# Kernel optimization log

Measured on AMD Instinct MI355X. Metric: run time of the kernel, lower is better.

Reference implementation:

```python
import jax, jax.numpy as jnp
import numpy as np

N, D, R, E, H = 100000, 128, 4, 150000, 8
DK = D // H  # 16


def setup_inputs() -> dict:
    key = jax.random.key(0)
    ks = jax.random.split(key, 12)
    w_scale = 1.0 / np.sqrt(D)
    rel_scale = 1.0 / np.sqrt(DK)
    return {
        'x': jax.random.normal(ks[0], (N, D), dtype=jnp.float32),
        'edges_src': jax.random.randint(ks[1], (R, E), 0, N, dtype=jnp.int32),
        'edges_dst': jax.random.randint(ks[2], (R, E), 0, N, dtype=jnp.int32),
        'Wk': jax.random.normal(ks[3], (D, D), dtype=jnp.float32) * w_scale,
        'bk': jnp.zeros((D,), dtype=jnp.float32),
        'Wq': jax.random.normal(ks[4], (D, D), dtype=jnp.float32) * w_scale,
        'bq': jnp.zeros((D,), dtype=jnp.float32),
        'Wv': jax.random.normal(ks[5], (D, D), dtype=jnp.float32) * w_scale,
        'bv': jnp.zeros((D,), dtype=jnp.float32),
        'Wa': jax.random.normal(ks[6], (D, D), dtype=jnp.float32) * w_scale,
        'ba': jnp.zeros((D,), dtype=jnp.float32),
        'rel_att': jax.random.normal(ks[7], (R, H, DK, DK), dtype=jnp.float32) * rel_scale,
        'rel_msg': jax.random.normal(ks[8], (R, H, DK, DK), dtype=jnp.float32) * rel_scale,
        'rel_pri': jnp.ones((R, H), dtype=jnp.float32),
        'skip': jnp.ones((1,), dtype=jnp.float32),
    }


def reference(x, edges_src, edges_dst, Wk, bk, Wq, bq, Wv, bv, Wa, ba,
              rel_att, rel_msg, rel_pri, skip):
    n, d = x.shape
    r, e = edges_src.shape
    h, dk = rel_att.shape[1], rel_att.shape[2]
    sqrt_dk = jnp.sqrt(jnp.asarray(dk, dtype=x.dtype))

    # per-type k/q/v projections (single node type) -> [N, H, dk]
    k = (x @ Wk.T + bk).reshape(n, h, dk)
    q = (x @ Wq.T + bq).reshape(n, h, dk)
    v = (x @ Wv.T + bv).reshape(n, h, dk)

    # edge_attention: per-relation per-head dk x dk transforms on gathered src feats
    key_e = jnp.einsum('rehd,rhdf->rehf', k[edges_src], rel_att)   # [R,E,H,dk]
    att = (q[edges_dst] * key_e).sum(-1) * rel_pri[:, None, :] / sqrt_dk  # [R,E,H]
    val = jnp.einsum('rehd,rhdf->rehf', v[edges_src], rel_msg)     # [R,E,H,dk]

    # mailbox softmax per (relation, dst node, head) via segment ops
    seg = (edges_dst.astype(jnp.int32) + jnp.arange(r, dtype=jnp.int32)[:, None] * n).reshape(-1)
    att_f = att.reshape(r * e, h)
    m = jax.ops.segment_max(att_f, seg, num_segments=r * n)
    a = jnp.exp(att_f - m[seg])
    s = jax.ops.segment_sum(a, seg, num_segments=r * n)
    attn = a / s[seg]                                              # [R*E, H]

    # softmax-weighted scatter aggregation -> [R, N, H*dk]
    msg = (attn[:, :, None] * val.reshape(r * e, h, dk)).reshape(r * e, h * dk)
    t = jax.ops.segment_sum(msg, seg, num_segments=r * n).reshape(r, n, d)
    t = t.mean(axis=0)  # cross_reducer='mean' over relations

    # skip-gated output linear (dropout is identity in eval)
    alpha = jax.nn.sigmoid(skip[0])
    return (t @ Wa.T + ba) * alpha + x * (1.0 - alpha)
```

## Files before the change

kernel.cpp:

```cpp
#include <hip/hip_runtime.h>

#define NN 100000
#define DD 128
#define RR 4
#define EE 150000
#define HH 8
#define DK 16

#define NSEG (RR * NN)
#define NEDGE (RR * EE)
#define SCAN_BLK 256
#define SCAN_ELEMS 1024
#define SCAN_NB ((NSEG + SCAN_ELEMS - 1) / SCAN_ELEMS)
#define PAD_K 136
#define MAT_U 132

typedef short bf16x8 __attribute__((ext_vector_type(8)));
typedef float f32x4  __attribute__((ext_vector_type(4)));

__device__ __forceinline__ unsigned short f2bf(float f) {
    unsigned u = __float_as_uint(f);
    return (unsigned short)((u + 0x7fffu + ((u >> 16) & 1u)) >> 16);
}
__device__ __forceinline__ float bflo(unsigned w) { return __uint_as_float(w << 16); }
__device__ __forceinline__ float bfhi(unsigned w) { return __uint_as_float(w & 0xffff0000u); }

__global__ __launch_bounds__(256) void mfma_qkv(
    const float* __restrict__ X,
    const float* __restrict__ Wq, const float* __restrict__ Wk, const float* __restrict__ Wv,
    const float* __restrict__ bq, const float* __restrict__ bk, const float* __restrict__ bv,
    float* __restrict__ qout, unsigned* __restrict__ kv)
{
    const int tid = threadIdx.x;
    const int lane = tid & 63;
    const int wave = tid >> 6;
    const int wr = wave >> 1;
    const int wc = wave & 1;
    const long m0 = (long)blockIdx.x * 64;
    const int mat = blockIdx.y;
    const float* W    = (mat == 0) ? Wq : (mat == 1) ? Wk : Wv;
    const float* bias = (mat == 0) ? bq : (mat == 1) ? bk : bv;

    __shared__ short Xs[64 * PAD_K];
    __shared__ short Wsh[128 * PAD_K];

    #pragma unroll
    for (int i = 0; i < 8; ++i) {
        int f = tid + 256 * i;
        int row = f >> 5, c4 = f & 31;
        long m = m0 + row;
        float4 v = make_float4(0.f, 0.f, 0.f, 0.f);
        if (m < NN) v = ((const float4*)(X + m * DD))[c4];
        unsigned u0 = (unsigned)f2bf(v.x) | ((unsigned)f2bf(v.y) << 16);
        unsigned u1 = (unsigned)f2bf(v.z) | ((unsigned)f2bf(v.w) << 16);
        *(uint2*)&Xs[row * PAD_K + c4 * 4] = make_uint2(u0, u1);
    }
    #pragma unroll
    for (int i = 0; i < 16; ++i) {
        int f = tid + 256 * i;
        int row = f >> 5, c4 = f & 31;
        float4 v = ((const float4*)(W + row * DD))[c4];
        unsigned u0 = (unsigned)f2bf(v.x) | ((unsigned)f2bf(v.y) << 16);
        unsigned u1 = (unsigned)f2bf(v.z) | ((unsigned)f2bf(v.w) << 16);
        *(uint2*)&Wsh[row * PAD_K + c4 * 4] = make_uint2(u0, u1);
    }
    __syncthreads();

    const int lrow = lane & 15;
    const int kg = lane >> 4;

    f32x4 acc[2][4];
    #pragma unroll
    for (int i = 0; i < 2; ++i)
        #pragma unroll
        for (int j = 0; j < 4; ++j) acc[i][j] = (f32x4){0.f, 0.f, 0.f, 0.f};

    #pragma unroll
    for (int ks = 0; ks < 4; ++ks) {
        const int kk = ks * 32 + kg * 8;
        bf16x8 xf[2], wf[4];
        #pragma unroll
        for (int i = 0; i < 2; ++i)
            xf[i] = *(const bf16x8*)&Xs[(wr * 32 + i * 16 + lrow) * PAD_K + kk];
        #pragma unroll
        for (int j = 0; j < 4; ++j)
            wf[j] = *(const bf16x8*)&Wsh[(wc * 64 + j * 16 + lrow) * PAD_K + kk];
        if (mat == 0) {
            #pragma unroll
            for (int i = 0; i < 2; ++i)
                #pragma unroll
                for (int j = 0; j < 4; ++j)
                    acc[i][j] = __builtin_amdgcn_mfma_f32_16x16x32_bf16(xf[i], wf[j], acc[i][j], 0, 0, 0);
        } else {
            #pragma unroll
            for (int i = 0; i < 2; ++i)
                #pragma unroll
                for (int j = 0; j < 4; ++j)
                    acc[i][j] = __builtin_amdgcn_mfma_f32_16x16x32_bf16(wf[j], xf[i], acc[i][j], 0, 0, 0);
        }
    }

    if (mat == 0) {
        #pragma unroll
        for (int j = 0; j < 4; ++j) {
            const int n = wc * 64 + j * 16 + lrow;
            const float bcol = bias[n];
            #pragma unroll
            for (int i = 0; i < 2; ++i) {
                #pragma unroll
                for (int r = 0; r < 4; ++r) {
                    long m = m0 + wr * 32 + i * 16 + kg * 4 + r;
                    if (m < NN) qout[m * DD + n] = acc[i][j][r] + bcol;
                }
            }
        }
    } else {
        const unsigned slotu = (mat == 1) ? 0u : 8u;
        #pragma unroll
        for (int j = 0; j < 4; ++j) {
            const int nb = wc * 64 + j * 16 + kg * 4;
            const float b0 = bias[nb + 0], b1 = bias[nb + 1];
            const float b2 = bias[nb + 2], b3 = bias[nb + 3];
            const int h = nb >> 4, d0 = nb & 15;
            #pragma unroll
            for (int i = 0; i < 2; ++i) {
                long m = m0 + wr * 32 + i * 16 + lrow;
                if (m < NN) {
                    unsigned u0 = (unsigned)f2bf(acc[i][j][0] + b0) | ((unsigned)f2bf(acc[i][j][1] + b1) << 16);
                    unsigned u1 = (unsigned)f2bf(acc[i][j][2] + b2) | ((unsigned)f2bf(acc[i][j][3] + b3) << 16);
                    *(uint2*)&kv[m * 128 + h * 16 + slotu + (d0 >> 1)] = make_uint2(u0, u1);
                }
            }
        }
    }
}

__global__ __launch_bounds__(256) void mfma_out(
    const float* __restrict__ T, const float* __restrict__ Wa, const float* __restrict__ ba,
    float* __restrict__ out, const float* __restrict__ skip, const float* __restrict__ xres)
{
    const int tid = threadIdx.x;
    const int lane = tid & 63;
    const int wave = tid >> 6;
    const int wr = wave >> 1;
    const int wc = wave & 1;
    const long m0 = (long)blockIdx.x * 64;

    __shared__ short Xs[64 * PAD_K];
    __shared__ short Wsh[128 * PAD_K];

    #pragma unroll
    for (int i = 0; i < 8; ++i) {
        int f = tid + 256 * i;
        int row = f >> 5, c4 = f & 31;
        long m = m0 + row;
        float4 v = make_float4(0.f, 0.f, 0.f, 0.f);
        if (m < NN) v = ((const float4*)(T + m * DD))[c4];
        unsigned u0 = (unsigned)f2bf(v.x * 0.25f) | ((unsigned)f2bf(v.y * 0.25f) << 16);
        unsigned u1 = (unsigned)f2bf(v.z * 0.25f) | ((unsigned)f2bf(v.w * 0.25f) << 16);
        *(uint2*)&Xs[row * PAD_K + c4 * 4] = make_uint2(u0, u1);
    }
    #pragma unroll
    for (int i = 0; i < 16; ++i) {
        int f = tid + 256 * i;
        int row = f >> 5, c4 = f & 31;
        float4 v = ((const float4*)(Wa + row * DD))[c4];
        unsigned u0 = (unsigned)f2bf(v.x) | ((unsigned)f2bf(v.y) << 16);
        unsigned u1 = (unsigned)f2bf(v.z) | ((unsigned)f2bf(v.w) << 16);
        *(uint2*)&Wsh[row * PAD_K + c4 * 4] = make_uint2(u0, u1);
    }
    __syncthreads();

    const int lrow = lane & 15;
    const int kg = lane >> 4;

    f32x4 acc[2][4];
    #pragma unroll
    for (int i = 0; i < 2; ++i)
        #pragma unroll
        for (int j = 0; j < 4; ++j) acc[i][j] = (f32x4){0.f, 0.f, 0.f, 0.f};

    #pragma unroll
    for (int ks = 0; ks < 4; ++ks) {
        const int kk = ks * 32 + kg * 8;
        bf16x8 xf[2], wf[4];
        #pragma unroll
        for (int i = 0; i < 2; ++i)
            xf[i] = *(const bf16x8*)&Xs[(wr * 32 + i * 16 + lrow) * PAD_K + kk];
        #pragma unroll
        for (int j = 0; j < 4; ++j)
            wf[j] = *(const bf16x8*)&Wsh[(wc * 64 + j * 16 + lrow) * PAD_K + kk];
        #pragma unroll
        for (int i = 0; i < 2; ++i)
            #pragma unroll
            for (int j = 0; j < 4; ++j)
                acc[i][j] = __builtin_amdgcn_mfma_f32_16x16x32_bf16(xf[i], wf[j], acc[i][j], 0, 0, 0);
    }

    const float s = 1.f / (1.f + __expf(-skip[0]));
    const float al = s, bt = 1.f - s;

    #pragma unroll
    for (int j = 0; j < 4; ++j) {
        const int n = wc * 64 + j * 16 + lrow;
        const float bcol = ba[n];
        #pragma unroll
        for (int i = 0; i < 2; ++i) {
            #pragma unroll
            for (int r = 0; r < 4; ++r) {
                long m = m0 + wr * 32 + i * 16 + kg * 4 + r;
                if (m < NN) {
                    long o = m * DD + n;
                    out[o] = __builtin_fmaf(xres[o], bt, (acc[i][j][r] + bcol) * al);
                }
            }
        }
    }
}


__global__ __launch_bounds__(256) void csr_hist(
    const int* __restrict__ edst, int* __restrict__ cnt)
{
    int idx = blockIdx.x * 256 + threadIdx.x;
    if (idx >= NEDGE) return;
    int r = idx / EE;
    atomicAdd(&cnt[r * NN + edst[idx]], 1);
}

__global__ __launch_bounds__(SCAN_BLK) void scan1(
    const int* __restrict__ cnt, int* __restrict__ offs, int* __restrict__ bsum)
{
    __shared__ int sh[SCAN_BLK];
    int blk = blockIdx.x, tid = threadIdx.x;
    int base = blk * SCAN_ELEMS + tid * 4;
    int v0 = 0, v1 = 0, v2 = 0, v3 = 0;
    if (base + 3 < NSEG) {
        int4 t = *(const int4*)(cnt + base);
        v0 = t.x; v1 = t.y; v2 = t.z; v3 = t.w;
    } else {
        if (base + 0 < NSEG) v0 = cnt[base + 0];
        if (base + 1 < NSEG) v1 = cnt[base + 1];
        if (base + 2 < NSEG) v2 = cnt[base + 2];
        if (base + 3 < NSEG) v3 = cnt[base + 3];
    }
    int tsum = v0 + v1 + v2 + v3;
    sh[tid] = tsum;
    __syncthreads();
    #pragma unroll
    for (int d = 1; d < SCAN_BLK; d <<= 1) {
        int x = (tid >= d) ? sh[tid - d] : 0;
        __syncthreads();
        sh[tid] += x;
        __syncthreads();
    }
    int excl = sh[tid] - tsum;
    int r0 = excl, r1 = r0 + v0, r2 = r1 + v1, r3 = r2 + v2;
    if (base + 3 < NSEG) {
        *(int4*)(offs + base) = make_int4(r0, r1, r2, r3);
    } else {
        if (base + 0 < NSEG) offs[base + 0] = r0;
        if (base + 1 < NSEG) offs[base + 1] = r1;
        if (base + 2 < NSEG) offs[base + 2] = r2;
        if (base + 3 < NSEG) offs[base + 3] = r3;
    }
    if (tid == SCAN_BLK - 1) bsum[blk] = sh[tid];
}

__global__ __launch_bounds__(512) void scan2(int* __restrict__ bsum)
{
    __shared__ int sh[512];
    int tid = threadIdx.x;
    int v = (tid < SCAN_NB) ? bsum[tid] : 0;
    sh[tid] = v;
    __syncthreads();
    #pragma unroll
    for (int d = 1; d < 512; d <<= 1) {
        int x = (tid >= d) ? sh[tid - d] : 0;
        __syncthreads();
        sh[tid] += x;
        __syncthreads();
    }
    if (tid < SCAN_NB) bsum[tid] = sh[tid] - v;
}

__global__ __launch_bounds__(SCAN_BLK) void scan3(
    int* __restrict__ offs, int* __restrict__ cur, const int* __restrict__ bsum)
{
    int blk = blockIdx.x;
    int add = bsum[blk];
    int base = blk * SCAN_ELEMS + threadIdx.x * 4;
    #pragma unroll
    for (int j = 0; j < 4; ++j)
        if (base + j < NSEG) {
            int v = offs[base + j] + add;
            offs[base + j] = v;
            cur[base + j] = v;
        }
}

__global__ __launch_bounds__(256) void csr_fill(
    const int* __restrict__ esrc, const int* __restrict__ edst,
    int* __restrict__ cur, int* __restrict__ csr_src)
{
    int idx = blockIdx.x * 256 + threadIdx.x;
    if (idx >= NEDGE) return;
    int r = idx / EE;
    int pos = atomicAdd(&cur[r * NN + edst[idx]], 1);
    csr_src[pos] = esrc[idx];
}

#define GT 512
__global__ __launch_bounds__(GT) void gather_agg(
    const unsigned* __restrict__ kv, const float* __restrict__ q,
    const int* __restrict__ csr_src, const int* __restrict__ offs,
    const float* __restrict__ rel_att, const float* __restrict__ rel_msg,
    const float* __restrict__ rel_pri, float* __restrict__ t)
{
    __shared__ unsigned As[32 * MAT_U];
    __shared__ unsigned Ms[32 * MAT_U];
    const int tid = threadIdx.x;
    #pragma unroll
    for (int i = 0; i < (32 * 128) / GT; ++i) {
        int f = tid + GT * i;
        int m = f >> 7, j = f & 127;
        float2 a = *(const float2*)(rel_att + m * 256 + j * 2);
        float2 b = *(const float2*)(rel_msg + m * 256 + j * 2);
        As[m * MAT_U + j] = (unsigned)f2bf(a.x) | ((unsigned)f2bf(a.y) << 16);
        Ms[m * MAT_U + j] = (unsigned)f2bf(b.x) | ((unsigned)f2bf(b.y) << 16);
    }
    __syncthreads();

    int gidx = blockIdx.x * GT + tid;
    if (gidx >= NN * HH) return;
    const int dst = gidx >> 3, h = gidx & 7;

    float qh[16];
    {
        const float4* qp = (const float4*)(q + (long)dst * DD + h * DK);
        #pragma unroll
        for (int i = 0; i < 4; ++i) {
            float4 a = qp[i];
            qh[4*i] = a.x; qh[4*i+1] = a.y; qh[4*i+2] = a.z; qh[4*i+3] = a.w;
        }
    }

    float tacc[16];
    #pragma unroll
    for (int f = 0; f < 16; ++f) tacc[f] = 0.f;

    for (int r = 0; r < RR; ++r) {
        const int seg = r * NN + dst;
        const int beg = offs[seg];
        const int end = (seg == NSEG - 1) ? NEDGE : offs[seg + 1];
        if (end <= beg) continue;

        const unsigned* A = &As[(r * HH + h) * MAT_U];
        const unsigned* M = &Ms[(r * HH + h) * MAT_U];
        const float pri = rel_pri[r * HH + h] * 0.25f;

        float qbar[16];
        #pragma unroll
        for (int d = 0; d < 16; ++d) {
            uint4 r0 = *(const uint4*)&A[d * 8];
            uint4 r1 = *(const uint4*)&A[d * 8 + 4];
            float acc = bflo(r0.x) * qh[0];
            acc = __builtin_fmaf(bfhi(r0.x), qh[1], acc);
            acc = __builtin_fmaf(bflo(r0.y), qh[2], acc);
            acc = __builtin_fmaf(bfhi(r0.y), qh[3], acc);
            acc = __builtin_fmaf(bflo(r0.z), qh[4], acc);
            acc = __builtin_fmaf(bfhi(r0.z), qh[5], acc);
            acc = __builtin_fmaf(bflo(r0.w), qh[6], acc);
            acc = __builtin_fmaf(bfhi(r0.w), qh[7], acc);
            acc = __builtin_fmaf(bflo(r1.x), qh[8], acc);
            acc = __builtin_fmaf(bfhi(r1.x), qh[9], acc);
            acc = __builtin_fmaf(bflo(r1.y), qh[10], acc);
            acc = __builtin_fmaf(bfhi(r1.y), qh[11], acc);
            acc = __builtin_fmaf(bflo(r1.z), qh[12], acc);
            acc = __builtin_fmaf(bfhi(r1.z), qh[13], acc);
            acc = __builtin_fmaf(bflo(r1.w), qh[14], acc);
            acc = __builtin_fmaf(bfhi(r1.w), qh[15], acc);
            qbar[d] = acc * pri;
        }

        float s = 0.f;
        float vb[16];
        #pragma unroll
        for (int f = 0; f < 16; ++f) vb[f] = 0.f;

        for (int e = beg; e < end; ++e) {
            int src = csr_src[e];
            const uint4* kvp = (const uint4*)kv + ((long)src * 32 + h * 4);
            uint4 ka = kvp[0], kb = kvp[1];
            uint4 va = kvp[2], vc = kvp[3];

            float att;
            att  = bflo(ka.x) * qbar[0];
            att = __builtin_fmaf(bfhi(ka.x), qbar[1], att);
            att = __builtin_fmaf(bflo(ka.y), qbar[2], att);
            att = __builtin_fmaf(bfhi(ka.y), qbar[3], att);
            att = __builtin_fmaf(bflo(ka.z), qbar[4], att);
            att = __builtin_fmaf(bfhi(ka.z), qbar[5], att);
            att = __builtin_fmaf(bflo(ka.w), qbar[6], att);
            att = __builtin_fmaf(bfhi(ka.w), qbar[7], att);
            att = __builtin_fmaf(bflo(kb.x), qbar[8], att);
            att = __builtin_fmaf(bfhi(kb.x), qbar[9], att);
            att = __builtin_fmaf(bflo(kb.y), qbar[10], att);
            att = __builtin_fmaf(bfhi(kb.y), qbar[11], att);
            att = __builtin_fmaf(bflo(kb.z), qbar[12], att);
            att = __builtin_fmaf(bfhi(kb.z), qbar[13], att);
            att = __builtin_fmaf(bflo(kb.w), qbar[14], att);
            att = __builtin_fmaf(bfhi(kb.w), qbar[15], att);

            float ea = __expf(att);
            s += ea;
            vb[0]  = __builtin_fmaf(ea, bflo(va.x), vb[0]);
            vb[1]  = __builtin_fmaf(ea, bfhi(va.x), vb[1]);
            vb[2]  = __builtin_fmaf(ea, bflo(va.y), vb[2]);
            vb[3]  = __builtin_fmaf(ea, bfhi(va.y), vb[3]);
            vb[4]  = __builtin_fmaf(ea, bflo(va.z), vb[4]);
            vb[5]  = __builtin_fmaf(ea, bfhi(va.z), vb[5]);
            vb[6]  = __builtin_fmaf(ea, bflo(va.w), vb[6]);
            vb[7]  = __builtin_fmaf(ea, bfhi(va.w), vb[7]);
            vb[8]  = __builtin_fmaf(ea, bflo(vc.x), vb[8]);
            vb[9]  = __builtin_fmaf(ea, bfhi(vc.x), vb[9]);
            vb[10] = __builtin_fmaf(ea, bflo(vc.y), vb[10]);
            vb[11] = __builtin_fmaf(ea, bfhi(vc.y), vb[11]);
            vb[12] = __builtin_fmaf(ea, bflo(vc.z), vb[12]);
            vb[13] = __builtin_fmaf(ea, bfhi(vc.z), vb[13]);
            vb[14] = __builtin_fmaf(ea, bflo(vc.w), vb[14]);
            vb[15] = __builtin_fmaf(ea, bfhi(vc.w), vb[15]);
        }

        float inv = 1.f / s;
        float u[16];
        #pragma unroll
        for (int f = 0; f < 16; ++f) u[f] = 0.f;
        #pragma unroll
        for (int d = 0; d < 16; ++d) {
            float vd = vb[d];
            uint4 m0 = *(const uint4*)&M[d * 8];
            uint4 m1 = *(const uint4*)&M[d * 8 + 4];
            u[0]  = __builtin_fmaf(vd, bflo(m0.x), u[0]);
            u[1]  = __builtin_fmaf(vd, bfhi(m0.x), u[1]);
            u[2]  = __builtin_fmaf(vd, bflo(m0.y), u[2]);
            u[3]  = __builtin_fmaf(vd, bfhi(m0.y), u[3]);
            u[4]  = __builtin_fmaf(vd, bflo(m0.z), u[4]);
            u[5]  = __builtin_fmaf(vd, bfhi(m0.z), u[5]);
            u[6]  = __builtin_fmaf(vd, bflo(m0.w), u[6]);
            u[7]  = __builtin_fmaf(vd, bfhi(m0.w), u[7]);
            u[8]  = __builtin_fmaf(vd, bflo(m1.x), u[8]);
            u[9]  = __builtin_fmaf(vd, bfhi(m1.x), u[9]);
            u[10] = __builtin_fmaf(vd, bflo(m1.y), u[10]);
            u[11] = __builtin_fmaf(vd, bfhi(m1.y), u[11]);
            u[12] = __builtin_fmaf(vd, bflo(m1.z), u[12]);
            u[13] = __builtin_fmaf(vd, bfhi(m1.z), u[13]);
            u[14] = __builtin_fmaf(vd, bflo(m1.w), u[14]);
            u[15] = __builtin_fmaf(vd, bfhi(m1.w), u[15]);
        }
        #pragma unroll
        for (int f = 0; f < 16; ++f)
            tacc[f] = __builtin_fmaf(u[f], inv, tacc[f]);
    }

    float* tp = t + (long)dst * DD + h * DK;
    #pragma unroll
    for (int i = 0; i < 4; ++i) {
        float4 o;
        o.x = tacc[4*i]; o.y = tacc[4*i+1]; o.z = tacc[4*i+2]; o.w = tacc[4*i+3];
        *(float4*)(tp + 4 * i) = o;
    }
}

extern "C" void kernel_launch(void* const* d_in, const int* in_sizes, int n_in,
                              void* d_out, int out_size, void* d_ws, size_t ws_size,
                              hipStream_t stream)
{
    const float* x   = (const float*)d_in[0];
    const int* esrc  = (const int*)d_in[1];
    const int* edst  = (const int*)d_in[2];
    const float* Wk  = (const float*)d_in[3];
    const float* bk  = (const float*)d_in[4];
    const float* Wq  = (const float*)d_in[5];
    const float* bq  = (const float*)d_in[6];
    const float* Wv  = (const float*)d_in[7];
    const float* bv  = (const float*)d_in[8];
    const float* Wa  = (const float*)d_in[9];
    const float* ba  = (const float*)d_in[10];
    const float* rel_att = (const float*)d_in[11];
    const float* rel_msg = (const float*)d_in[12];
    const float* rel_pri = (const float*)d_in[13];
    const float* skip    = (const float*)d_in[14];
    float* out = (float*)d_out;

    float* ws = (float*)d_ws;
    const long ND = (long)NN * DD;
    float* qbuf = ws;
    float* tbuf = ws + ND;
    unsigned* kvb = (unsigned*)(ws + 2 * ND);
    int* cnt  = (int*)(ws + 3 * ND);
    int* offs = cnt + NSEG;
    int* cur  = offs + NSEG;
    int* bsum = cur + NSEG;
    int* csr  = bsum + 512;

    hipMemsetAsync(cnt, 0, NSEG * sizeof(int), stream);

    const int gb = (NN + 63) / 64;
    mfma_qkv<<<dim3(gb, 3), 256, 0, stream>>>(x, Wq, Wk, Wv, bq, bk, bv, qbuf, kvb);

    const int ebk = (NEDGE + 255) / 256;
    csr_hist<<<ebk, 256, 0, stream>>>(edst, cnt);
    scan1<<<SCAN_NB, SCAN_BLK, 0, stream>>>(cnt, offs, bsum);
    scan2<<<1, 512, 0, stream>>>(bsum);
    scan3<<<SCAN_NB, SCAN_BLK, 0, stream>>>(offs, cur, bsum);
    csr_fill<<<ebk, 256, 0, stream>>>(esrc, edst, cur, csr);

    gather_agg<<<(NN * HH + GT - 1) / GT, GT, 0, stream>>>(
        kvb, qbuf, csr, offs, rel_att, rel_msg, rel_pri, tbuf);

    mfma_out<<<gb, 256, 0, stream>>>(tbuf, Wa, ba, out, skip, x);
}
```

Baseline: 365.7 us.

## Fold per-relation message transforms into V projection weights, store q as bf16

Precomputes four per-relation fused weight matrices Wm = rel_msg^T·Wv (plus fused biases) in a small prep kernel. The projection GEMM then emits K, Q and four relation-specific transformed V tensors in bf16. The gather kernel no longer applies the 16x16 message matrix per destination, and it reads q as bf16 instead of fp32. In exchange the projection does twice the GEMM work and writes four V buffers instead of one, so the per-edge V reads hit a larger, less cache-friendly footprint spread across relations.

```diff
diff --git a/kernel.cpp b/kernel.cpp
--- a/kernel.cpp
+++ b/kernel.cpp
@@ -14,6 +14,7 @@
 #define SCAN_NB ((NSEG + SCAN_ELEMS - 1) / SCAN_ELEMS)
 #define PAD_K 136
 #define MAT_U 132
+#define ND2 (NN * 64)
 
 typedef short bf16x8 __attribute__((ext_vector_type(8)));
 typedef float f32x4  __attribute__((ext_vector_type(4)));
@@ -25,11 +26,40 @@
 __device__ __forceinline__ float bflo(unsigned w) { return __uint_as_float(w << 16); }
 __device__ __forceinline__ float bfhi(unsigned w) { return __uint_as_float(w & 0xffff0000u); }
 
-__global__ __launch_bounds__(256) void mfma_qkv(
+__global__ __launch_bounds__(128) void prep_wmsg(
+    const float* __restrict__ Wv, const float* __restrict__ bv,
+    const float* __restrict__ rel_msg,
+    float* __restrict__ Wm, float* __restrict__ bm)
+{
+    const int b = blockIdx.x;
+    const int r = b >> 3, h = b & 7;
+    const int c = threadIdx.x;
+    __shared__ float Msh[256];
+    for (int i = c; i < 256; i += 128) Msh[i] = rel_msg[(b << 8) + i];
+    __syncthreads();
+
+    #pragma unroll 4
+    for (int f = 0; f < 16; ++f) {
+        float acc = 0.f;
+        #pragma unroll
+        for (int d = 0; d < 16; ++d)
+            acc = __builtin_fmaf(Msh[d * 16 + f], Wv[(h * 16 + d) * DD + c], acc);
+        Wm[((long)r * DD + h * 16 + f) * DD + c] = acc;
+    }
+    if (c < 16) {
+        float acc = 0.f;
+        #pragma unroll
+        for (int d = 0; d < 16; ++d)
+            acc = __builtin_fmaf(Msh[d * 16 + c], bv[h * 16 + d], acc);
+        bm[r * DD + h * 16 + c] = acc;
+    }
+}
+
+__global__ __launch_bounds__(256) void mfma_proj(
     const float* __restrict__ X,
-    const float* __restrict__ Wq, const float* __restrict__ Wk, const float* __restrict__ Wv,
-    const float* __restrict__ bq, const float* __restrict__ bk, const float* __restrict__ bv,
-    float* __restrict__ qout, unsigned* __restrict__ kv)
+    const float* __restrict__ Wk, const float* __restrict__ Wq, const float* __restrict__ Wm,
+    const float* __restrict__ bk, const float* __restrict__ bq, const float* __restrict__ bm,
+    unsigned* __restrict__ kb, unsigned* __restrict__ qb, unsigned* __restrict__ vMb)
 {
     const int tid = threadIdx.x;
     const int lane = tid & 63;
@@ -38,8 +68,9 @@
     const int wc = wave & 1;
     const long m0 = (long)blockIdx.x * 64;
     const int mat = blockIdx.y;
-    const float* W    = (mat == 0) ? Wq : (mat == 1) ? Wk : Wv;
-    const float* bias = (mat == 0) ? bq : (mat == 1) ? bk : bv;
+    const float* W    = (mat == 0) ? Wk : (mat == 1) ? Wq : (Wm + (long)(mat - 2) * DD * DD);
+    const float* bias = (mat == 0) ? bk : (mat == 1) ? bq : (bm + (mat - 2) * DD);
+    unsigned* out     = (mat == 0) ? kb : (mat == 1) ? qb : (vMb + (long)(mat - 2) * ND2);
 
     __shared__ short Xs[64 * PAD_K];
     __shared__ short Wsh[128 * PAD_K];
@@ -85,51 +116,25 @@
         #pragma unroll
         for (int j = 0; j < 4; ++j)
             wf[j] = *(const bf16x8*)&Wsh[(wc * 64 + j * 16 + lrow) * PAD_K + kk];
-        if (mat == 0) {
+        #pragma unroll
+        for (int i = 0; i < 2; ++i)
             #pragma unroll
-            for (int i = 0; i < 2; ++i)
-                #pragma unroll
-                for (int j = 0; j < 4; ++j)
-                    acc[i][j] = __builtin_amdgcn_mfma_f32_16x16x32_bf16(xf[i], wf[j], acc[i][j], 0, 0, 0);
-        } else {
-            #pragma unroll
-            for (int i = 0; i < 2; ++i)
-                #pragma unroll
-                for (int j = 0; j < 4; ++j)
-                    acc[i][j] = __builtin_amdgcn_mfma_f32_16x16x32_bf16(wf[j], xf[i], acc[i][j], 0, 0, 0);
-        }
-    }
-
-    if (mat == 0) {
-        #pragma unroll
-        for (int j = 0; j < 4; ++j) {
-            const int n = wc * 64 + j * 16 + lrow;
-            const float bcol = bias[n];
-            #pragma unroll
-            for (int i = 0; i < 2; ++i) {
-                #pragma unroll
-                for (int r = 0; r < 4; ++r) {
-                    long m = m0 + wr * 32 + i * 16 + kg * 4 + r;
-                    if (m < NN) qout[m * DD + n] = acc[i][j][r] + bcol;
-                }
-            }
-        }
-    } else {
-        const unsigned slotu = (mat == 1) ? 0u : 8u;
-        #pragma unroll
-        for (int j = 0; j < 4; ++j) {
-            const int nb = wc * 64 + j * 16 + kg * 4;
-            const float b0 = bias[nb + 0], b1 = bias[nb + 1];
-            const float b2 = bias[nb + 2], b3 = bias[nb + 3];
-            const int h = nb >> 4, d0 = nb & 15;
-            #pragma unroll
-            for (int i = 0; i < 2; ++i) {
-                long m = m0 + wr * 32 + i * 16 + lrow;
-                if (m < NN) {
-                    unsigned u0 = (unsigned)f2bf(acc[i][j][0] + b0) | ((unsigned)f2bf(acc[i][j][1] + b1) << 16);
-                    unsigned u1 = (unsigned)f2bf(acc[i][j][2] + b2) | ((unsigned)f2bf(acc[i][j][3] + b3) << 16);
-                    *(uint2*)&kv[m * 128 + h * 16 + slotu + (d0 >> 1)] = make_uint2(u0, u1);
-                }
+            for (int j = 0; j < 4; ++j)
+                acc[i][j] = __builtin_amdgcn_mfma_f32_16x16x32_bf16(wf[j], xf[i], acc[i][j], 0, 0, 0);
+    }
+
+    #pragma unroll
+    for (int j = 0; j < 4; ++j) {
+        const int nb = wc * 64 + j * 16 + kg * 4;
+        const float b0 = bias[nb + 0], b1 = bias[nb + 1];
+        const float b2 = bias[nb + 2], b3 = bias[nb + 3];
+        #pragma unroll
+        for (int i = 0; i < 2; ++i) {
+            long m = m0 + wr * 32 + i * 16 + lrow;
+            if (m < NN) {
+                unsigned u0 = (unsigned)f2bf(acc[i][j][0] + b0) | ((unsigned)f2bf(acc[i][j][1] + b1) << 16);
+                unsigned u1 = (unsigned)f2bf(acc[i][j][2] + b2) | ((unsigned)f2bf(acc[i][j][3] + b3) << 16);
+                *(uint2*)&out[m * 64 + (nb >> 1)] = make_uint2(u0, u1);
             }
         }
     }
@@ -312,23 +317,23 @@
 
 #define GT 512
 __global__ __launch_bounds__(GT) void gather_agg(
-    const unsigned* __restrict__ kv, const float* __restrict__ q,
+    const unsigned* __restrict__ kb, const unsigned* __restrict__ qbuf,
+    const unsigned* __restrict__ vMb,
     const int* __restrict__ csr_src, const int* __restrict__ offs,
-    const float* __restrict__ rel_att, const float* __restrict__ rel_msg,
-    const float* __restrict__ rel_pri, float* __restrict__ t)
+    const float* __restrict__ rel_att, const float* __restrict__ rel_pri,
+    float* __restrict__ t)
 {
     __shared__ unsigned As[32 * MAT_U];
-    __shared__ unsigned Ms[32 * MAT_U];
+    __shared__ float prish[32];
     const int tid = threadIdx.x;
     #pragma unroll
     for (int i = 0; i < (32 * 128) / GT; ++i) {
         int f = tid + GT * i;
         int m = f >> 7, j = f & 127;
         float2 a = *(const float2*)(rel_att + m * 256 + j * 2);
-        float2 b = *(const float2*)(rel_msg + m * 256 + j * 2);
         As[m * MAT_U + j] = (unsigned)f2bf(a.x) | ((unsigned)f2bf(a.y) << 16);
-        Ms[m * MAT_U + j] = (unsigned)f2bf(b.x) | ((unsigned)f2bf(b.y) << 16);
-    }
+    }
+    if (tid < 32) prish[tid] = rel_pri[tid] * 0.25f;
     __syncthreads();
 
     int gidx = blockIdx.x * GT + tid;
@@ -337,12 +342,16 @@
 
     float qh[16];
     {
-        const float4* qp = (const float4*)(q + (long)dst * DD + h * DK);
-        #pragma unroll
-        for (int i = 0; i < 4; ++i) {
-            float4 a = qp[i];
-            qh[4*i] = a.x; qh[4*i+1] = a.y; qh[4*i+2] = a.z; qh[4*i+3] = a.w;
-        }
+        const uint4* qp = (const uint4*)(qbuf + (long)dst * 64 + h * 8);
+        uint4 qa = qp[0], qc = qp[1];
+        qh[0] = bflo(qa.x);  qh[1] = bfhi(qa.x);
+        qh[2] = bflo(qa.y);  qh[3] = bfhi(qa.y);
+        qh[4] = bflo(qa.z);  qh[5] = bfhi(qa.z);
+        qh[6] = bflo(qa.w);  qh[7] = bfhi(qa.w);
+        qh[8] = bflo(qc.x);  qh[9] = bfhi(qc.x);
+        qh[10] = bflo(qc.y); qh[11] = bfhi(qc.y);
+        qh[12] = bflo(qc.z); qh[13] = bfhi(qc.z);
+        qh[14] = bflo(qc.w); qh[15] = bfhi(qc.w);
     }
 
     float tacc[16];
@@ -356,8 +365,7 @@
         if (end <= beg) continue;
 
         const unsigned* A = &As[(r * HH + h) * MAT_U];
-        const unsigned* M = &Ms[(r * HH + h) * MAT_U];
-        const float pri = rel_pri[r * HH + h] * 0.25f;
+        const float pri = prish[r * HH + h];
 
         float qbar[16];
         #pragma unroll
@@ -388,11 +396,13 @@
         #pragma unroll
         for (int f = 0; f < 16; ++f) vb[f] = 0.f;
 
+        const unsigned* vMr = vMb + (long)r * ND2;
         for (int e = beg; e < end; ++e) {
             int src = csr_src[e];
-            const uint4* kvp = (const uint4*)kv + ((long)src * 32 + h * 4);
-            uint4 ka = kvp[0], kb = kvp[1];
-            uint4 va = kvp[2], vc = kvp[3];
+            const uint4* kp = (const uint4*)(kb + (long)src * 64 + h * 8);
+            uint4 ka = kp[0], kc = kp[1];
+            const uint4* vp = (const uint4*)(vMr + (long)src * 64 + h * 8);
+            uint4 va = vp[0], vc = vp[1];
 
             float att;
             att  = bflo(ka.x) * qbar[0];
@@ -403,14 +413,14 @@
             att = __builtin_fmaf(bfhi(ka.z), qbar[5], att);
             att = __builtin_fmaf(bflo(ka.w), qbar[6], att);
             att = __builtin_fmaf(bfhi(ka.w), qbar[7], att);
-            att = __builtin_fmaf(bflo(kb.x), qbar[8], att);
-            att = __builtin_fmaf(bfhi(kb.x), qbar[9], att);
-            att = __builtin_fmaf(bflo(kb.y), qbar[10], att);
-            att = __builtin_fmaf(bfhi(kb.y), qbar[11], att);
-            att = __builtin_fmaf(bflo(kb.z), qbar[12], att);
-            att = __builtin_fmaf(bfhi(kb.z), qbar[13], att);
-            att = __builtin_fmaf(bflo(kb.w), qbar[14], att);
-            att = __builtin_fmaf(bfhi(kb.w), qbar[15], att);
+            att = __builtin_fmaf(bflo(kc.x), qbar[8], att);
+            att = __builtin_fmaf(bfhi(kc.x), qbar[9], att);
+            att = __builtin_fmaf(bflo(kc.y), qbar[10], att);
+            att = __builtin_fmaf(bfhi(kc.y), qbar[11], att);
+            att = __builtin_fmaf(bflo(kc.z), qbar[12], att);
+            att = __builtin_fmaf(bfhi(kc.z), qbar[13], att);
+            att = __builtin_fmaf(bflo(kc.w), qbar[14], att);
+            att = __builtin_fmaf(bfhi(kc.w), qbar[15], att);
 
             float ea = __expf(att);
             s += ea;
@@ -433,34 +443,9 @@
         }
 
         float inv = 1.f / s;
-        float u[16];
-        #pragma unroll
-        for (int f = 0; f < 16; ++f) u[f] = 0.f;
-        #pragma unroll
-        for (int d = 0; d < 16; ++d) {
-            float vd = vb[d];
-            uint4 m0 = *(const uint4*)&M[d * 8];
-            uint4 m1 = *(const uint4*)&M[d * 8 + 4];
-            u[0]  = __builtin_fmaf(vd, bflo(m0.x), u[0]);
-            u[1]  = __builtin_fmaf(vd, bfhi(m0.x), u[1]);
-            u[2]  = __builtin_fmaf(vd, bflo(m0.y), u[2]);
-            u[3]  = __builtin_fmaf(vd, bfhi(m0.y), u[3]);
-            u[4]  = __builtin_fmaf(vd, bflo(m0.z), u[4]);
-            u[5]  = __builtin_fmaf(vd, bfhi(m0.z), u[5]);
-            u[6]  = __builtin_fmaf(vd, bflo(m0.w), u[6]);
-            u[7]  = __builtin_fmaf(vd, bfhi(m0.w), u[7]);
-            u[8]  = __builtin_fmaf(vd, bflo(m1.x), u[8]);
-            u[9]  = __builtin_fmaf(vd, bfhi(m1.x), u[9]);
-            u[10] = __builtin_fmaf(vd, bflo(m1.y), u[10]);
-            u[11] = __builtin_fmaf(vd, bfhi(m1.y), u[11]);
-            u[12] = __builtin_fmaf(vd, bflo(m1.z), u[12]);
-            u[13] = __builtin_fmaf(vd, bfhi(m1.z), u[13]);
-            u[14] = __builtin_fmaf(vd, bflo(m1.w), u[14]);
-            u[15] = __builtin_fmaf(vd, bfhi(m1.w), u[15]);
-        }
         #pragma unroll
         for (int f = 0; f < 16; ++f)
-            tacc[f] = __builtin_fmaf(u[f], inv, tacc[f]);
+            tacc[f] = __builtin_fmaf(vb[f], inv, tacc[f]);
     }
 
     float* tp = t + (long)dst * DD + h * DK;
@@ -495,10 +480,13 @@
 
     float* ws = (float*)d_ws;
     const long ND = (long)NN * DD;
-    float* qbuf = ws;
-    float* tbuf = ws + ND;
-    unsigned* kvb = (unsigned*)(ws + 2 * ND);
-    int* cnt  = (int*)(ws + 3 * ND);
+    float* tbuf = ws;
+    unsigned* qb  = (unsigned*)(ws + ND);
+    unsigned* kb  = qb + ND2;
+    unsigned* vMb = kb + ND2;
+    float* Wm = (float*)(vMb + 4L * ND2);
+    float* bm = Wm + 4 * DD * DD;
+    int* cnt  = (int*)(bm + 512);
     int* offs = cnt + NSEG;
     int* cur  = offs + NSEG;
     int* bsum = cur + NSEG;
@@ -506,8 +494,10 @@
 
     hipMemsetAsync(cnt, 0, NSEG * sizeof(int), stream);
 
+    prep_wmsg<<<32, 128, 0, stream>>>(Wv, bv, rel_msg, Wm, bm);
+
     const int gb = (NN + 63) / 64;
-    mfma_qkv<<<dim3(gb, 3), 256, 0, stream>>>(x, Wq, Wk, Wv, bq, bk, bv, qbuf, kvb);
+    mfma_proj<<<dim3(gb, 6), 256, 0, stream>>>(x, Wk, Wq, Wm, bk, bq, bm, kb, qb, vMb);
 
     const int ebk = (NEDGE + 255) / 256;
     csr_hist<<<ebk, 256, 0, stream>>>(edst, cnt);
@@ -517,7 +507,7 @@
     csr_fill<<<ebk, 256, 0, stream>>>(esrc, edst, cur, csr);
 
     gather_agg<<<(NN * HH + GT - 1) / GT, GT, 0, stream>>>(
-        kvb, qbuf, csr, offs, rel_att, rel_msg, rel_pri, tbuf);
+        kb, qb, vMb, csr, offs, rel_att, rel_pri, tbuf);
 
     mfma_out<<<gb, 256, 0, stream>>>(tbuf, Wa, ba, out, skip, x);
 }
```

Measured after the change: 335.2 us. 8.3% less time.
